# Optimization experiments

Hardware: AMD Instinct MI355X
Metric: run time of the kernel (lower is better)

The kernel has to match this reference:

```python
import jax, jax.numpy as jnp
import numpy as np
import math

B, C, S, O, K = 64, 271, 512, 512, 32  # seq_len S must equal out_channels O (einsum constraint in original)

def setup_inputs() -> dict:
    key = jax.random.key(0)
    k1, k2, k3, k4, k5 = jax.random.split(key, 5)
    x = jax.random.normal(k1, (B, C, S), dtype=jnp.float32)
    fourier_features = jax.random.normal(k2, (O, K, K, 4), dtype=jnp.float32)
    sensor_positions = jax.random.uniform(k3, (C, 2), dtype=jnp.float32)
    proj_w = jax.random.normal(k4, (O, C), dtype=jnp.float32) / np.float32(math.sqrt(C))
    proj_b = jax.random.normal(k5, (O,), dtype=jnp.float32) * 0.02
    return {"x": x, "fourier_features": fourier_features,
            "sensor_positions": sensor_positions, "proj_w": proj_w, "proj_b": proj_b}

def reference(x, fourier_features, sensor_positions, proj_w, proj_b):
    Kdim = fourier_features.shape[1]
    freqs = 2.0 * jnp.pi * jnp.arange(Kdim, dtype=jnp.float32) / Kdim
    # meshgrid(freqs_x, freqs_y, indexing='ij') stacked on last dim -> [K,K,2]
    grid = jnp.stack(jnp.meshgrid(freqs, freqs, indexing='ij'), axis=-1)
    # feature map is batch-independent: [C,K,K,2] -> sin/cos cat -> [C,K,K,4]
    fm = sensor_positions[:, None, None, :] * grid[None]
    fm = jnp.concatenate([jnp.sin(fm), jnp.cos(fm)], axis=-1)
    # attention logits [O,C]; original expands over batch but result is identical per batch
    att = jnp.einsum('ckhw,okhw->oc', fm, fourier_features)
    att = jax.nn.softmax(att, axis=0)  # softmax over out_channels (dim=1 of [B,O,C])
    # 1x1 Conv1d: [B,C,S] -> [B,O,S]
    xp = jnp.einsum('bcs,oc->bos', x, proj_w) + proj_b[None, :, None]
    # original: einsum('bci,bio->bco', xp[B,O,S], attn[B,O,C]); contraction over S(==O)
    out = jnp.einsum('bps,sq->bpq', xp, att)  # [B,O,C]
    return out
```

## Files before the change

kernel.cpp:

```cpp
#include <hip/hip_runtime.h>
#include <hip/hip_bf16.h>
#include <math.h>


typedef short s16x8 __attribute__((ext_vector_type(8)));
typedef short s16x4 __attribute__((ext_vector_type(4)));
typedef float f32x4 __attribute__((ext_vector_type(4)));

#define GLOBAL_AS __attribute__((address_space(1)))
#define LDS_AS    __attribute__((address_space(3)))

__device__ __forceinline__ short f2bf(float f) {
    __hip_bfloat16 h = __float2bfloat16(f);
    return *reinterpret_cast<short*>(&h);
}

#define Cdim 271
#define CpK  288
#define Sdim 512
#define Odim 512
#define MF   17344
#define MFp  17408

__global__ __launch_bounds__(512) void gemm7(
    const float* __restrict__ x,
    const short* __restrict__ BT,
    short* __restrict__ yT)
{
    const int m0 = blockIdx.x * 128;
    const int n0 = blockIdx.y * 128;
    __shared__ short pool[24576];

    const int t = threadIdx.x;
    const int lane = t & 63;
    const int wid = t >> 6;
    const int wr = wid >> 2;
    const int wc = wid & 3;
    const int lr = lane & 15, lkq = lane >> 4;

    f32x4 acc[4][2];
    #pragma unroll
    for (int i = 0; i < 4; ++i)
        #pragma unroll
        for (int j = 0; j < 2; ++j)
            acc[i][j] = (f32x4){0.f, 0.f, 0.f, 0.f};

    const int srowB = wid * 16 + (lane >> 2);
    const int skk   = (((lane & 3) ^ ((lane >> 3) & 3)) * 8);
    const short* pB = BT + (long)(n0 + srowB) * Sdim + skk;
    const int ldsOff = wid * 512;

    const int arow = t >> 2;
    const int aslot = t & 3;
    const int afc = (aslot ^ ((arow >> 1) & 3)) * 8;
    const int agrow = (m0 + arow < MF) ? (m0 + arow) : (MF - 1);
    const float* pA_f32 = x + (long)agrow * Sdim + afc;
    const int aWr = arow * 32 + aslot * 8;

    const int kxs = ((lkq ^ ((lr >> 1) & 3)) << 3);
    const int aBase = (wr * 64 + lr) * 32 + kxs;
    const int bBase = (wc * 32 + lr) * 32 + kxs;

    auto stageB = [&](int buf, int kt) {
        __builtin_amdgcn_global_load_lds((const GLOBAL_AS void*)(pB + kt * 32),
            (LDS_AS void*)&pool[12288 + buf * 4096 + ldsOff], 16, 0, 0);
    };
    auto compute = [&](int buf) {
        s16x8 af[4], bfv[2];
        #pragma unroll
        for (int m = 0; m < 4; ++m)
            af[m] = *(const s16x8*)&pool[buf * 4096 + aBase + m * 512];
        #pragma unroll
        for (int n = 0; n < 2; ++n)
            bfv[n] = *(const s16x8*)&pool[12288 + buf * 4096 + bBase + n * 512];
        #pragma unroll
        for (int m = 0; m < 4; ++m)
            #pragma unroll
            for (int n = 0; n < 2; ++n)
                acc[m][n] = __builtin_amdgcn_mfma_f32_16x16x32_bf16(af[m], bfv[n], acc[m][n], 0, 0, 0);
    };

    const int nk = Sdim / 32;
    f32x4 aP0, aP1, aN0, aN1;
    auto loadA = [&](int kt, f32x4& v0, f32x4& v1) {
        const float* p = pA_f32 + kt * 32;
        v0 = *(const f32x4 GLOBAL_AS*)(p);
        v1 = *(const f32x4 GLOBAL_AS*)(p + 4);
    };
    auto writeA = [&](int buf, const f32x4& v0, const f32x4& v1) {
        s16x8 w;
        #pragma unroll
        for (int j = 0; j < 4; ++j) { w[j] = f2bf(v0[j]); w[4 + j] = f2bf(v1[j]); }
        *(s16x8*)&pool[buf * 4096 + aWr] = w;
    };
    loadA(0, aP0, aP1); stageB(0, 0);
    writeA(0, aP0, aP1);
    loadA(1, aP0, aP1); stageB(1, 1);
    int bc = 0, bs = 2;
    for (int kt = 0; kt < nk; ++kt) {
        if (kt + 1 < nk) asm volatile("s_waitcnt vmcnt(3) lgkmcnt(0)" ::: "memory");
        else             asm volatile("s_waitcnt vmcnt(0) lgkmcnt(0)" ::: "memory");
        __builtin_amdgcn_s_barrier();
        __builtin_amdgcn_sched_barrier(0);
        if (kt + 2 < nk) { loadA(kt + 2, aN0, aN1); stageB(bs, kt + 2); }
        compute(bc);
        if (kt + 1 < nk) writeA((bc == 2) ? 0 : bc + 1, aP0, aP1);
        aP0 = aN0; aP1 = aN1;
        bc = (bc == 2) ? 0 : bc + 1;
        bs = (bs == 2) ? 0 : bs + 1;
    }

    __syncthreads();
    short* T = pool;
    #pragma unroll
    for (int i = 0; i < 4; ++i) {
        const int ml = wr * 64 + i * 16 + lkq * 4;
        #pragma unroll
        for (int j = 0; j < 2; ++j) {
            const int ql = wc * 32 + j * 16 + lr;
            s16x4 v;
            #pragma unroll
            for (int r = 0; r < 4; ++r) v[r] = f2bf(acc[i][j][r]);
            *(s16x4*)&T[ql * 132 + ml] = v;
        }
    }
    __syncthreads();
    short* Oy = yT;
    #pragma unroll
    for (int p = 0; p < 4; ++p) {
        const int ql = p * 32 + (t >> 4);
        const int gq = n0 + ql;
        const int mlc = (t & 15) * 8;
        const s16x8 v = *(const s16x8*)&T[ql * 132 + mlc];
        const int gm0 = m0 + mlc;
        if (gq < Cdim && gm0 < MF) {
            const int b0 = gm0 / Cdim;
            const int c0 = gm0 - b0 * Cdim;
            if (c0 + 8 <= Cdim) {
                *(s16x8*)&Oy[((long)b0 * Cdim + gq) * CpK + c0] = v;
            } else {
                #pragma unroll
                for (int r = 0; r < 8; ++r) {
                    const int gm = gm0 + r;
                    if (gm < MF) {
                        const int bb = gm / Cdim;
                        const int cc = gm - bb * Cdim;
                        Oy[((long)bb * Cdim + gq) * CpK + cc] = v[r];
                    }
                }
            }
        }
    }
}

__global__ __launch_bounds__(512) void gemm8w(
    const short* __restrict__ A,
    const short* __restrict__ BT,
    float* __restrict__ O,
    const float* __restrict__ bias)
{
    const int m0 = blockIdx.y * 256;
    const int n0 = blockIdx.x * 128;
    __shared__ short pool[36864];

    const int t = threadIdx.x;
    const int lane = t & 63;
    const int wid = t >> 6;
    const int wr = wid >> 1;
    const int wc = wid & 1;
    const int lr = lane & 15, lkq = lane >> 4;

    f32x4 acc[4][4];
    #pragma unroll
    for (int i = 0; i < 4; ++i)
        #pragma unroll
        for (int j = 0; j < 4; ++j)
            acc[i][j] = (f32x4){0.f, 0.f, 0.f, 0.f};

    const int srow = wid * 16 + (lane >> 2);
    const int skk  = (((lane & 3) ^ ((lane >> 3) & 3)) * 8);
    const short* pA0 = A + (long)(m0 + srow) * CpK + skk;
    const short* pA1 = A + (long)(m0 + 128 + srow) * CpK + skk;
    const short* pB  = BT + (long)(n0 + srow) * CpK + skk;
    const int ldsOff = wid * 512;

    const int kxs = ((lkq ^ ((lr >> 1) & 3)) << 3);
    const int aBase = (wr * 64 + lr) * 32 + kxs;
    const int bBase = (wc * 64 + lr) * 32 + kxs;

    auto stage = [&](int buf, int kt) {
        __builtin_amdgcn_global_load_lds((const GLOBAL_AS void*)(pA0 + kt * 32),
            (LDS_AS void*)&pool[buf * 8192 + ldsOff], 16, 0, 0);
        __builtin_amdgcn_global_load_lds((const GLOBAL_AS void*)(pA1 + kt * 32),
            (LDS_AS void*)&pool[buf * 8192 + 4096 + ldsOff], 16, 0, 0);
        __builtin_amdgcn_global_load_lds((const GLOBAL_AS void*)(pB + kt * 32),
            (LDS_AS void*)&pool[24576 + buf * 4096 + ldsOff], 16, 0, 0);
    };
    auto compute = [&](int buf) {
        s16x8 af[4], bfv[4];
        #pragma unroll
        for (int m = 0; m < 4; ++m)
            af[m] = *(const s16x8*)&pool[buf * 8192 + aBase + m * 512];
        #pragma unroll
        for (int n = 0; n < 4; ++n)
            bfv[n] = *(const s16x8*)&pool[24576 + buf * 4096 + bBase + n * 512];
        #pragma unroll
        for (int m = 0; m < 4; ++m)
            #pragma unroll
            for (int n = 0; n < 4; ++n)
                acc[m][n] = __builtin_amdgcn_mfma_f32_16x16x32_bf16(af[m], bfv[n], acc[m][n], 0, 0, 0);
    };

    const int nk = CpK / 32;
    stage(0, 0); stage(1, 1);
    int bc = 0, bs = 2;
    for (int kt = 0; kt < nk; ++kt) {
        if (kt + 1 < nk) asm volatile("s_waitcnt vmcnt(3)" ::: "memory");
        else             asm volatile("s_waitcnt vmcnt(0)" ::: "memory");
        __builtin_amdgcn_s_barrier();
        __builtin_amdgcn_sched_barrier(0);
        if (kt + 2 < nk) stage(bs, kt + 2);
        compute(bc);
        bc = (bc == 2) ? 0 : bc + 1;
        bs = (bs == 2) ? 0 : bs + 1;
    }

    #pragma unroll
    for (int j = 0; j < 4; ++j) {
        const int gn = n0 + wc * 64 + j * 16 + lr;
        if (gn >= MF) continue;
        const int b = gn / Cdim;
        const int q = gn - b * Cdim;
        float* ob = O + (long)b * Odim * Cdim + q;
        #pragma unroll
        for (int i = 0; i < 4; ++i) {
            const int gmb = m0 + wr * 64 + i * 16 + lkq * 4;
            #pragma unroll
            for (int r = 0; r < 4; ++r) {
                const int gm = gmb + r;
                ob[(long)gm * Cdim] = acc[i][j][r] + bias[gm];
            }
        }
    }
}

__global__ __launch_bounds__(256) void ff_reduce(const float* __restrict__ ff,
                                                 float* __restrict__ GT)
{
    __shared__ float L[2][32 * 132];
    const int t = threadIdx.x;
    const int half = t >> 7;
    const int tl = t & 127;
    const int o = blockIdx.x * 2 + half;
    const float* base = ff + (long)o * 4096;
    #pragma unroll
    for (int ch = 0; ch < 8; ++ch) {
        const int g = ch * 512 + tl * 4;
        const f32x4 v = *(const f32x4*)&base[g];
        *(f32x4*)&L[half][(g >> 7) * 132 + (g & 127)] = v;
    }
    __syncthreads();
    const int gq = tl >> 5, idx = tl & 31;
    float s = 0.f;
    if (gq == 0 || gq == 2) {
        const int w = (gq == 0) ? 0 : 2;
        #pragma unroll 8
        for (int j = 0; j < 32; ++j) s += L[half][idx * 132 + j * 4 + w];
    } else {
        const int w = (gq == 1) ? 1 : 3;
        #pragma unroll 8
        for (int i = 0; i < 32; ++i) s += L[half][i * 132 + idx * 4 + w];
    }
    GT[tl * 512 + o] = s;
}

__device__ __forceinline__ float wave_max(float v) {
    #pragma unroll
    for (int off = 32; off; off >>= 1) v = fmaxf(v, __shfl_xor(v, off));
    return v;
}
__device__ __forceinline__ float wave_sum(float v) {
    #pragma unroll
    for (int off = 32; off; off >>= 1) v += __shfl_xor(v, off);
    return v;
}

__global__ __launch_bounds__(512) void att4(
    const float* __restrict__ GT,
    const float* __restrict__ sp,
    short* __restrict__ attT,
    const float* __restrict__ pw,
    short* __restrict__ pwb)
{
    const int blk = blockIdx.x;
    const int t = threadIdx.x;
    if (blk >= 68) {
        const int bi = blk - 68;
        const int idx8 = (bi * 512 + t) * 8;
        const int p = idx8 / CpK;
        const int k0 = idx8 - p * CpK;
        s16x8 v;
        #pragma unroll
        for (int r = 0; r < 8; ++r) {
            const int k = k0 + r;
            v[r] = (k < Cdim) ? f2bf(pw[(long)p * Cdim + k]) : (short)0;
        }
        *(s16x8*)&pwb[idx8] = v;
        return;
    }

    const int c0 = blk * 4;
    __shared__ float u[4][128];
    __shared__ float red[32];
    {
        const int ci = t >> 7, k = t & 127;
        const int csafe = (c0 + ci < Cdim) ? (c0 + ci) : (Cdim - 1);
        const int g = k >> 5, kk = k & 31;
        const float f = 6.283185307179586477f * (float)kk / 32.0f;
        const float p = sp[csafe * 2 + (g & 1)];
        const float ang = p * f;
        u[ci][k] = (g < 2) ? sinf(ang) : cosf(ang);
    }
    __syncthreads();

    float l[4] = {0.f, 0.f, 0.f, 0.f};
    #pragma unroll 8
    for (int k = 0; k < 128; ++k) {
        const float g = GT[k * 512 + t];
        #pragma unroll
        for (int ci = 0; ci < 4; ++ci) l[ci] = fmaf(g, u[ci][k], l[ci]);
    }

    const int lane = t & 63, wid = t >> 6;
    float m[4];
    #pragma unroll
    for (int ci = 0; ci < 4; ++ci) m[ci] = wave_max(l[ci]);
    if (lane == 0) {
        #pragma unroll
        for (int ci = 0; ci < 4; ++ci) red[wid * 4 + ci] = m[ci];
    }
    __syncthreads();
    #pragma unroll
    for (int ci = 0; ci < 4; ++ci) {
        float mm = red[ci];
        #pragma unroll
        for (int w = 1; w < 8; ++w) mm = fmaxf(mm, red[w * 4 + ci]);
        m[ci] = mm;
    }
    __syncthreads();
    float e[4], s[4];
    #pragma unroll
    for (int ci = 0; ci < 4; ++ci) { e[ci] = expf(l[ci] - m[ci]); s[ci] = wave_sum(e[ci]); }
    if (lane == 0) {
        #pragma unroll
        for (int ci = 0; ci < 4; ++ci) red[wid * 4 + ci] = s[ci];
    }
    __syncthreads();
    #pragma unroll
    for (int ci = 0; ci < 4; ++ci) {
        float ss = red[ci];
        #pragma unroll
        for (int w = 1; w < 8; ++w) ss += red[w * 4 + ci];
        const int c = c0 + ci;
        if (c < Cdim) attT[(long)c * Sdim + t] = f2bf(e[ci] / ss);
    }
}

extern "C" void kernel_launch(void* const* d_in, const int* in_sizes, int n_in,
                              void* d_out, int out_size, void* d_ws, size_t ws_size,
                              hipStream_t stream)
{
    const float* x  = (const float*)d_in[0];
    const float* ff = (const float*)d_in[1];
    const float* sp = (const float*)d_in[2];
    const float* pw = (const float*)d_in[3];
    const float* pb = (const float*)d_in[4];
    float* out = (float*)d_out;

    float* ws   = (float*)d_ws;
    float* GT   = ws;
    short* attT = (short*)(GT + 128 * 512);
    short* pwb  = attT + 384L * Sdim;
    short* yT   = pwb + (long)Odim * CpK;

    ff_reduce<<<256, 256, 0, stream>>>(ff, GT);
    att4<<<104, 512, 0, stream>>>(GT, sp, attT, pw, pwb);

    gemm7<<<dim3(MFp / 128, 3), 512, 0, stream>>>(x, attT, yT);

    gemm8w<<<dim3(MFp / 128, Odim / 256), 512, 0, stream>>>(pwb, yT, out, pb);
}
```

Measured before the change: 58.62 us.

## Deepen GEMM pipelines to four stages and shrink second GEMM tile to 128x128

Both GEMM kernels move from a three-buffer to a four-buffer LDS ring with three tiles in flight, with the waitcnt thresholds adjusted to match and launch bounds hinting at four blocks per CU. The second GEMM also drops from 256x128 to 128x128 tiles with fewer accumulators per wave, which doubles its grid. The aim is to hide more global-load latency and raise occupancy. The cost is more LDS per block in gemm7, less data reuse per tile, and more redundant loads of the shared operand in the second GEMM.

```diff
diff --git a/kernel.cpp b/kernel.cpp
--- a/kernel.cpp
+++ b/kernel.cpp
@@ -22,14 +22,14 @@
 #define MF   17344
 #define MFp  17408
 
-__global__ __launch_bounds__(512) void gemm7(
+__global__ __launch_bounds__(512, 4) void gemm7(
     const float* __restrict__ x,
     const short* __restrict__ BT,
     short* __restrict__ yT)
 {
     const int m0 = blockIdx.x * 128;
     const int n0 = blockIdx.y * 128;
-    __shared__ short pool[24576];
+    __shared__ short pool[32768];
 
     const int t = threadIdx.x;
     const int lane = t & 63;
@@ -63,7 +63,7 @@
 
     auto stageB = [&](int buf, int kt) {
         __builtin_amdgcn_global_load_lds((const GLOBAL_AS void*)(pB + kt * 32),
-            (LDS_AS void*)&pool[12288 + buf * 4096 + ldsOff], 16, 0, 0);
+            (LDS_AS void*)&pool[16384 + buf * 4096 + ldsOff], 16, 0, 0);
     };
     auto compute = [&](int buf) {
         s16x8 af[4], bfv[2];
@@ -72,7 +72,7 @@
             af[m] = *(const s16x8*)&pool[buf * 4096 + aBase + m * 512];
         #pragma unroll
         for (int n = 0; n < 2; ++n)
-            bfv[n] = *(const s16x8*)&pool[12288 + buf * 4096 + bBase + n * 512];
+            bfv[n] = *(const s16x8*)&pool[16384 + buf * 4096 + bBase + n * 512];
         #pragma unroll
         for (int m = 0; m < 4; ++m)
             #pragma unroll
@@ -81,7 +81,7 @@
     };
 
     const int nk = Sdim / 32;
-    f32x4 aP0, aP1, aN0, aN1;
+    f32x4 P0, P1, Q0, Q1, N0, N1;
     auto loadA = [&](int kt, f32x4& v0, f32x4& v1) {
         const float* p = pA_f32 + kt * 32;
         v0 = *(const f32x4 GLOBAL_AS*)(p);
@@ -93,21 +93,21 @@
         for (int j = 0; j < 4; ++j) { w[j] = f2bf(v0[j]); w[4 + j] = f2bf(v1[j]); }
         *(s16x8*)&pool[buf * 4096 + aWr] = w;
     };
-    loadA(0, aP0, aP1); stageB(0, 0);
-    writeA(0, aP0, aP1);
-    loadA(1, aP0, aP1); stageB(1, 1);
-    int bc = 0, bs = 2;
+    loadA(0, P0, P1); stageB(0, 0);
+    writeA(0, P0, P1);
+    loadA(1, P0, P1); stageB(1, 1);
+    loadA(2, Q0, Q1); stageB(2, 2);
     for (int kt = 0; kt < nk; ++kt) {
-        if (kt + 1 < nk) asm volatile("s_waitcnt vmcnt(3) lgkmcnt(0)" ::: "memory");
-        else             asm volatile("s_waitcnt vmcnt(0) lgkmcnt(0)" ::: "memory");
+        const int rem = nk - 1 - kt;
+        if (rem >= 2)      asm volatile("s_waitcnt vmcnt(4) lgkmcnt(0)" ::: "memory");
+        else if (rem == 1) asm volatile("s_waitcnt vmcnt(2) lgkmcnt(0)" ::: "memory");
+        else               asm volatile("s_waitcnt vmcnt(0) lgkmcnt(0)" ::: "memory");
         __builtin_amdgcn_s_barrier();
         __builtin_amdgcn_sched_barrier(0);
-        if (kt + 2 < nk) { loadA(kt + 2, aN0, aN1); stageB(bs, kt + 2); }
-        compute(bc);
-        if (kt + 1 < nk) writeA((bc == 2) ? 0 : bc + 1, aP0, aP1);
-        aP0 = aN0; aP1 = aN1;
-        bc = (bc == 2) ? 0 : bc + 1;
-        bs = (bs == 2) ? 0 : bs + 1;
+        if (kt + 3 < nk) { loadA(kt + 3, N0, N1); stageB((kt + 3) & 3, kt + 3); }
+        compute(kt & 3);
+        if (kt + 1 < nk) writeA((kt + 1) & 3, P0, P1);
+        P0 = Q0; P1 = Q1; Q0 = N0; Q1 = N1;
     }
 
     __syncthreads();
@@ -153,81 +153,77 @@
     }
 }
 
-__global__ __launch_bounds__(512) void gemm8w(
+__global__ __launch_bounds__(512, 4) void gemm8k(
     const short* __restrict__ A,
     const short* __restrict__ BT,
     float* __restrict__ O,
     const float* __restrict__ bias)
 {
-    const int m0 = blockIdx.y * 256;
+    const int m0 = blockIdx.y * 128;
     const int n0 = blockIdx.x * 128;
-    __shared__ short pool[36864];
+    __shared__ short pool[32768];
 
     const int t = threadIdx.x;
     const int lane = t & 63;
     const int wid = t >> 6;
-    const int wr = wid >> 1;
-    const int wc = wid & 1;
+    const int wr = wid >> 2;
+    const int wc = wid & 3;
     const int lr = lane & 15, lkq = lane >> 4;
 
-    f32x4 acc[4][4];
+    f32x4 acc[4][2];
     #pragma unroll
     for (int i = 0; i < 4; ++i)
         #pragma unroll
-        for (int j = 0; j < 4; ++j)
+        for (int j = 0; j < 2; ++j)
             acc[i][j] = (f32x4){0.f, 0.f, 0.f, 0.f};
 
     const int srow = wid * 16 + (lane >> 2);
     const int skk  = (((lane & 3) ^ ((lane >> 3) & 3)) * 8);
-    const short* pA0 = A + (long)(m0 + srow) * CpK + skk;
-    const short* pA1 = A + (long)(m0 + 128 + srow) * CpK + skk;
-    const short* pB  = BT + (long)(n0 + srow) * CpK + skk;
+    const short* pA = A + (long)(m0 + srow) * CpK + skk;
+    const short* pB = BT + (long)(n0 + srow) * CpK + skk;
     const int ldsOff = wid * 512;
 
     const int kxs = ((lkq ^ ((lr >> 1) & 3)) << 3);
     const int aBase = (wr * 64 + lr) * 32 + kxs;
-    const int bBase = (wc * 64 + lr) * 32 + kxs;
+    const int bBase = (wc * 32 + lr) * 32 + kxs;
 
     auto stage = [&](int buf, int kt) {
-        __builtin_amdgcn_global_load_lds((const GLOBAL_AS void*)(pA0 + kt * 32),
-            (LDS_AS void*)&pool[buf * 8192 + ldsOff], 16, 0, 0);
-        __builtin_amdgcn_global_load_lds((const GLOBAL_AS void*)(pA1 + kt * 32),
-            (LDS_AS void*)&pool[buf * 8192 + 4096 + ldsOff], 16, 0, 0);
+        __builtin_amdgcn_global_load_lds((const GLOBAL_AS void*)(pA + kt * 32),
+            (LDS_AS void*)&pool[buf * 4096 + ldsOff], 16, 0, 0);
         __builtin_amdgcn_global_load_lds((const GLOBAL_AS void*)(pB + kt * 32),
-            (LDS_AS void*)&pool[24576 + buf * 4096 + ldsOff], 16, 0, 0);
+            (LDS_AS void*)&pool[16384 + buf * 4096 + ldsOff], 16, 0, 0);
     };
     auto compute = [&](int buf) {
-        s16x8 af[4], bfv[4];
+        s16x8 af[4], bfv[2];
         #pragma unroll
         for (int m = 0; m < 4; ++m)
-            af[m] = *(const s16x8*)&pool[buf * 8192 + aBase + m * 512];
-        #pragma unroll
-        for (int n = 0; n < 4; ++n)
-            bfv[n] = *(const s16x8*)&pool[24576 + buf * 4096 + bBase + n * 512];
+            af[m] = *(const s16x8*)&pool[buf * 4096 + aBase + m * 512];
+        #pragma unroll
+        for (int n = 0; n < 2; ++n)
+            bfv[n] = *(const s16x8*)&pool[16384 + buf * 4096 + bBase + n * 512];
         #pragma unroll
         for (int m = 0; m < 4; ++m)
             #pragma unroll
-            for (int n = 0; n < 4; ++n)
+            for (int n = 0; n < 2; ++n)
                 acc[m][n] = __builtin_amdgcn_mfma_f32_16x16x32_bf16(af[m], bfv[n], acc[m][n], 0, 0, 0);
     };
 
     const int nk = CpK / 32;
-    stage(0, 0); stage(1, 1);
-    int bc = 0, bs = 2;
+    stage(0, 0); stage(1, 1); stage(2, 2);
     for (int kt = 0; kt < nk; ++kt) {
-        if (kt + 1 < nk) asm volatile("s_waitcnt vmcnt(3)" ::: "memory");
-        else             asm volatile("s_waitcnt vmcnt(0)" ::: "memory");
+        const int rem = nk - 1 - kt;
+        if (rem >= 2)      asm volatile("s_waitcnt vmcnt(4)" ::: "memory");
+        else if (rem == 1) asm volatile("s_waitcnt vmcnt(2)" ::: "memory");
+        else               asm volatile("s_waitcnt vmcnt(0)" ::: "memory");
         __builtin_amdgcn_s_barrier();
         __builtin_amdgcn_sched_barrier(0);
-        if (kt + 2 < nk) stage(bs, kt + 2);
-        compute(bc);
-        bc = (bc == 2) ? 0 : bc + 1;
-        bs = (bs == 2) ? 0 : bs + 1;
-    }
-
-    #pragma unroll
-    for (int j = 0; j < 4; ++j) {
-        const int gn = n0 + wc * 64 + j * 16 + lr;
+        if (kt + 3 < nk) stage((kt + 3) & 3, kt + 3);
+        compute(kt & 3);
+    }
+
+    #pragma unroll
+    for (int j = 0; j < 2; ++j) {
+        const int gn = n0 + wc * 32 + j * 16 + lr;
         if (gn >= MF) continue;
         const int b = gn / Cdim;
         const int q = gn - b * Cdim;
@@ -388,5 +384,5 @@
 
     gemm7<<<dim3(MFp / 128, 3), 512, 0, stream>>>(x, attT, yT);
 
-    gemm8w<<<dim3(MFp / 128, Odim / 256), 512, 0, stream>>>(pwb, yT, out, pb);
-}
+    gemm8k<<<dim3(MFp / 128, Odim / 128), 512, 0, stream>>>(pwb, yT, out, pb);
+}
```

Measured after the change: 56.83 us (median of 3 runs). 3.1% less time.
